# Kernel tuning notes

Hardware: AMD Instinct MI355X
Metric: run time of the kernel (lower is better)

The kernel has to match this reference:

```python
import jax, jax.numpy as jnp
import numpy as np

N, E, G = 50000, 800000, 64
IN, HID, HEADS, OUT = 128, 64, 4, 128
NEG = 0.2  # PyG GATConv default negative_slope


def setup_inputs() -> dict:
    key = jax.random.key(0)
    ks = jax.random.split(key, 12)
    nrm = lambda k, shape, s: (jax.random.normal(k, shape, jnp.float32) * s)
    x = nrm(ks[0], (N, IN), 1.0)
    edge_index = jax.random.randint(ks[1], (2, E), 0, N)
    batch = jnp.sort(jax.random.randint(ks[2], (N,), 0, G))
    W1 = nrm(ks[3], (IN, HEADS * HID), IN ** -0.5)
    a1_src = nrm(ks[4], (HEADS, HID), HID ** -0.5)
    a1_dst = nrm(ks[5], (HEADS, HID), HID ** -0.5)
    b1 = jnp.zeros((HEADS * HID,), jnp.float32)
    W2 = nrm(ks[6], (HEADS * HID, OUT), (HEADS * HID) ** -0.5)
    a2_src = nrm(ks[7], (1, OUT), OUT ** -0.5)
    a2_dst = nrm(ks[8], (1, OUT), OUT ** -0.5)
    b2 = jnp.zeros((OUT,), jnp.float32)
    fc_W = nrm(ks[9], (OUT, OUT), OUT ** -0.5)
    fc_b = jnp.zeros((OUT,), jnp.float32)
    return dict(x=x, edge_index=edge_index, batch=batch, W1=W1, a1_src=a1_src,
                a1_dst=a1_dst, b1=b1, W2=W2, a2_src=a2_src, a2_dst=a2_dst,
                b2=b2, fc_W=fc_W, fc_b=fc_b)


def gat_conv(x, W, a_src, a_dst, b, src, dst, heads):
    n = x.shape[0]
    ch = W.shape[1] // heads
    h = (x @ W).reshape(n, heads, ch)                      # [n, H, C]
    al_s = jnp.einsum('nhc,hc->nh', h, a_src)              # per-node src logits
    al_d = jnp.einsum('nhc,hc->nh', h, a_dst)
    e = al_s[src] + al_d[dst]                              # [E, H]
    e = jnp.where(e > 0, e, NEG * e)                       # LeakyReLU
    # segment softmax over incoming edges of each dst node
    m = jax.lax.stop_gradient(jax.ops.segment_max(e, dst, num_segments=n))
    m = jnp.where(jnp.isfinite(m), m, 0.0)
    ex = jnp.exp(e - m[dst])
    s = jax.ops.segment_sum(ex, dst, num_segments=n)
    alpha = ex / (s[dst] + 1e-16)                          # [E, H]
    out = jax.ops.segment_sum(h[src] * alpha[..., None], dst, num_segments=n)
    return out.reshape(n, heads * ch) + b                  # concat heads + bias


def reference(x, edge_index, batch, W1, a1_src, a1_dst, b1, W2, a2_src, a2_dst, b2, fc_W, fc_b):
    loops = jnp.arange(N, dtype=edge_index.dtype)          # PyG adds self-loops
    src = jnp.concatenate([edge_index[0], loops])
    dst = jnp.concatenate([edge_index[1], loops])
    h = jax.nn.elu(gat_conv(x, W1, a1_src, a1_dst, b1, src, dst, HEADS))
    h = jax.nn.elu(gat_conv(h, W2, a2_src, a2_dst, b2, src, dst, 1))
    sums = jax.ops.segment_sum(h, batch, num_segments=G)
    cnt = jax.ops.segment_sum(jnp.ones((N,), h.dtype), batch, num_segments=G)
    pooled = sums / jnp.maximum(cnt, 1.0)[:, None]         # global mean pool
    return jax.nn.relu(pooled @ fc_W + fc_b)
```

## Files before the change

kernel.cpp:

```cpp
#include <hip/hip_runtime.h>
#include <math.h>

#define N_NODES 50000
#define N_EDGES 800000
#define N_GRAPHS 64
#define NEG 0.2f

typedef unsigned short us;
typedef us us2 __attribute__((ext_vector_type(2)));
typedef us us4 __attribute__((ext_vector_type(4)));
typedef us us8 __attribute__((ext_vector_type(8)));
typedef short bf16x8 __attribute__((ext_vector_type(8)));
typedef float f32x4 __attribute__((ext_vector_type(4)));

__device__ __forceinline__ us bf16rn(float f) {
  unsigned int u = __float_as_uint(f);
  u += 0x7FFFu + ((u >> 16) & 1u);
  return (us)(u >> 16);
}
__device__ __forceinline__ float bf2f(us h) {
  return __uint_as_float(((unsigned int)h) << 16);
}

__global__ __launch_bounds__(256) void convW_kernel(
    const float* __restrict__ W1, const float* __restrict__ W2,
    us* __restrict__ w1h, us* __restrict__ w1l,
    us* __restrict__ w2h, us* __restrict__ w2l) {
  int idx = blockIdx.x * 256 + threadIdx.x;
  const float* W; us *oh, *ol; int K, N, li;
  if (idx < 128 * 256) {
    W = W1; oh = w1h; ol = w1l; K = 128; N = 256; li = idx;
  } else if (idx < 2 * 128 * 256) {
    W = W2; oh = w2h; ol = w2l; K = 256; N = 128; li = idx - 128 * 256;
  } else return;
  int n = li / K, k = li - n * K;
  float f = W[(size_t)k * N + n];
  us h = bf16rn(f);
  oh[li] = h;
  ol[li] = bf16rn(f - bf2f(h));
}

__global__ __launch_bounds__(256, 2) void gemm_bf16x3(
    const float* __restrict__ A, const us* __restrict__ Bth,
    const us* __restrict__ Btl, us* __restrict__ C, int M, int N, int K) {
  __shared__ us Ah[128][40];
  __shared__ us Al[128][40];
  __shared__ us Bh[128][40];
  __shared__ us Bl[128][40];
  int t = threadIdx.x;
  int m0 = blockIdx.x * 128;
  int n0 = blockIdx.y * 128;
  int w = t >> 6, l = t & 63;
  int wr = w >> 1, wc = w & 1;
  int l15 = l & 15, g = l >> 4;

  f32x4 acc[4][4] = {};

  for (int kb = 0; kb < K; kb += 32) {
    #pragma unroll
    for (int i = 0; i < 4; i++) {
      int slot = i * 256 + t;
      int row = slot >> 3, kq = slot & 7;
      float4 v = make_float4(0.f, 0.f, 0.f, 0.f);
      if (m0 + row < M) v = *(const float4*)&A[(size_t)(m0 + row) * K + kb + kq * 4];
      us h0 = bf16rn(v.x), h1 = bf16rn(v.y), h2 = bf16rn(v.z), h3 = bf16rn(v.w);
      us4 hv = {h0, h1, h2, h3};
      us4 lv = {bf16rn(v.x - bf2f(h0)), bf16rn(v.y - bf2f(h1)),
                bf16rn(v.z - bf2f(h2)), bf16rn(v.w - bf2f(h3))};
      *(us4*)&Ah[row][kq * 4] = hv;
      *(us4*)&Al[row][kq * 4] = lv;
    }
    #pragma unroll
    for (int i = 0; i < 2; i++) {
      int slot = i * 256 + t;
      int n = slot >> 2, kq = slot & 3;
      size_t gidx = (size_t)(n0 + n) * K + kb + kq * 8;
      *(us8*)&Bh[n][kq * 8] = *(const us8*)&Bth[gidx];
      *(us8*)&Bl[n][kq * 8] = *(const us8*)&Btl[gidx];
    }
    __syncthreads();

    bf16x8 af[4], al4[4], bf[4], bl4[4];
    #pragma unroll
    for (int i = 0; i < 4; i++) {
      af[i]  = *(const bf16x8*)&Ah[wr * 64 + i * 16 + l15][g * 8];
      al4[i] = *(const bf16x8*)&Al[wr * 64 + i * 16 + l15][g * 8];
      bf[i]  = *(const bf16x8*)&Bh[wc * 64 + i * 16 + l15][g * 8];
      bl4[i] = *(const bf16x8*)&Bl[wc * 64 + i * 16 + l15][g * 8];
    }
    #pragma unroll
    for (int i = 0; i < 4; i++)
      #pragma unroll
      for (int j = 0; j < 4; j++) {
        acc[i][j] = __builtin_amdgcn_mfma_f32_16x16x32_bf16(af[i], bf[j], acc[i][j], 0, 0, 0);
        acc[i][j] = __builtin_amdgcn_mfma_f32_16x16x32_bf16(af[i], bl4[j], acc[i][j], 0, 0, 0);
        acc[i][j] = __builtin_amdgcn_mfma_f32_16x16x32_bf16(al4[i], bf[j], acc[i][j], 0, 0, 0);
      }
    __syncthreads();
  }

  #pragma unroll
  for (int i = 0; i < 4; i++)
    #pragma unroll
    for (int j = 0; j < 4; j++)
      #pragma unroll
      for (int r = 0; r < 4; r++) {
        int row = m0 + wr * 64 + i * 16 + g * 4 + r;
        if (row < M) {
          int col = n0 + wc * 64 + j * 16 + l15;
          C[(size_t)row * N + col] = bf16rn(acc[i][j][r]);
        }
      }
}

__global__ __launch_bounds__(256) void logits1_kernel(
    const us* __restrict__ h1b, const float* __restrict__ a_src,
    const float* __restrict__ a_dst, float* __restrict__ al_s,
    float* __restrict__ al_d) {
  int idx = blockIdx.x * 256 + threadIdx.x;
  if (idx >= N_NODES * 4) return;
  int n = idx >> 2, h = idx & 3;
  const us* hp = &h1b[(size_t)n * 256 + h * 64];
  float ss = 0.f, sd = 0.f;
  #pragma unroll
  for (int i = 0; i < 8; i++) {
    us8 v = *(const us8*)&hp[i * 8];
    #pragma unroll
    for (int j = 0; j < 8; j++) {
      float f = bf2f(v[j]);
      ss += f * a_src[h * 64 + i * 8 + j];
      sd += f * a_dst[h * 64 + i * 8 + j];
    }
  }
  al_s[idx] = ss;
  al_d[idx] = sd;
}

__global__ __launch_bounds__(256) void logits2_kernel(
    const us* __restrict__ h2b, const float* __restrict__ a_src,
    const float* __restrict__ a_dst, float* __restrict__ al_s,
    float* __restrict__ al_d) {
  int n = blockIdx.x * 256 + threadIdx.x;
  if (n >= N_NODES) return;
  const us* hp = &h2b[(size_t)n * 128];
  float ss = 0.f, sd = 0.f;
  #pragma unroll
  for (int i = 0; i < 16; i++) {
    us8 v = *(const us8*)&hp[i * 8];
    #pragma unroll
    for (int j = 0; j < 8; j++) {
      float f = bf2f(v[j]);
      ss += f * a_src[i * 8 + j];
      sd += f * a_dst[i * 8 + j];
    }
  }
  al_s[n] = ss;
  al_d[n] = sd;
}

__global__ __launch_bounds__(256) void count_kernel(const int* __restrict__ dst,
                                                    int* __restrict__ cnt) {
  int e = blockIdx.x * 256 + threadIdx.x;
  if (e < N_EDGES) atomicAdd(&cnt[dst[e]], 1);
}

__global__ __launch_bounds__(256) void scan1_kernel(const int* __restrict__ cnt,
                                                    int* __restrict__ itmp,
                                                    int* __restrict__ bsum) {
  int i = blockIdx.x * 256 + threadIdx.x;
  int v = (i < N_NODES) ? cnt[i] : 0;
  int lane = threadIdx.x & 63, w = threadIdx.x >> 6;
  int s = v;
  #pragma unroll
  for (int off = 1; off < 64; off <<= 1) {
    int tv = __shfl_up(s, off);
    if (lane >= off) s += tv;
  }
  __shared__ int wsum[4];
  if (lane == 63) wsum[w] = s;
  __syncthreads();
  int add = 0;
  for (int p = 0; p < w; p++) add += wsum[p];
  s += add;
  if (i < N_NODES) itmp[i] = s;
  if (threadIdx.x == 255) bsum[blockIdx.x] = s;
}

__global__ __launch_bounds__(256) void scan2_kernel(const int* __restrict__ bsum,
                                                    int* __restrict__ boff,
                                                    int nb) {
  int t = threadIdx.x;
  int v = (t < nb) ? bsum[t] : 0;
  int lane = t & 63, w = t >> 6;
  int s = v;
  #pragma unroll
  for (int off = 1; off < 64; off <<= 1) {
    int tv = __shfl_up(s, off);
    if (lane >= off) s += tv;
  }
  __shared__ int wsum[4];
  if (lane == 63) wsum[w] = s;
  __syncthreads();
  int add = 0;
  for (int p = 0; p < w; p++) add += wsum[p];
  s += add;
  if (t < nb) boff[t] = s - v;
}

__global__ __launch_bounds__(256) void scan3_kernel(const int* __restrict__ cnt,
                                                    const int* __restrict__ itmp,
                                                    const int* __restrict__ boff,
                                                    int* __restrict__ rowst,
                                                    int* __restrict__ cursor) {
  int i = blockIdx.x * 256 + threadIdx.x;
  if (i < N_NODES) {
    int excl = itmp[i] - cnt[i] + boff[i >> 8];
    rowst[i] = excl;
    cursor[i] = excl;
  }
  if (i == 0) rowst[N_NODES] = N_EDGES;
}

__global__ __launch_bounds__(256) void scatter_kernel(
    const int* __restrict__ src, const int* __restrict__ dst,
    int* __restrict__ cursor, int* __restrict__ csr_src) {
  int e = blockIdx.x * 256 + threadIdx.x;
  if (e < N_EDGES) {
    int p = atomicAdd(&cursor[dst[e]], 1);
    csr_src[p] = src[e];
  }
}

__global__ __launch_bounds__(256) void agg1_kernel(
    const us* __restrict__ h1b, const float* __restrict__ al_s,
    const float* __restrict__ al_d, const int* __restrict__ rowst,
    const int* __restrict__ csrc, const float* __restrict__ b1,
    float* __restrict__ out) {
  int d = (blockIdx.x * 256 + threadIdx.x) >> 6;
  int lane = threadIdx.x & 63;
  if (d >= N_NODES) return;
  int head = lane >> 4;
  int c0 = lane * 4;
  int wsel = lane & 48;
  float ald = al_d[d * 4 + head];
  float wsum = 0.f, a0 = 0.f, a1 = 0.f, a2 = 0.f, a3 = 0.f;
  {
    float v = al_s[d * 4 + head] + ald;
    v = v > 0.f ? v : NEG * v;
    float w = __expf(v);
    us4 hv = *(const us4*)&h1b[(size_t)d * 256 + c0];
    wsum += w;
    a0 += w * bf2f(hv[0]); a1 += w * bf2f(hv[1]);
    a2 += w * bf2f(hv[2]); a3 += w * bf2f(hv[3]);
  }
  int beg = rowst[d], end = rowst[d + 1];
  for (int j = beg; j < end; j += 16) {
    int m = end - j;
    m = m < 16 ? m : 16;
    int el = lane & 15;
    int sv = csrc[j + (el < m ? el : 0)];
    float v = al_s[sv * 4 + head] + ald;
    v = v > 0.f ? v : NEG * v;
    float wv = __expf(v);
    #pragma unroll 4
    for (int k = 0; k < m; ++k) {
      int s = __shfl(sv, k);
      float w = __shfl(wv, k + wsel);
      us4 hv = *(const us4*)&h1b[(size_t)s * 256 + c0];
      wsum += w;
      a0 += w * bf2f(hv[0]); a1 += w * bf2f(hv[1]);
      a2 += w * bf2f(hv[2]); a3 += w * bf2f(hv[3]);
    }
  }
  float inv = 1.f / (wsum + 1e-16f);
  float4 bb = *(const float4*)&b1[c0];
  float o0 = a0 * inv + bb.x, o1 = a1 * inv + bb.y;
  float o2 = a2 * inv + bb.z, o3 = a3 * inv + bb.w;
  o0 = o0 > 0.f ? o0 : expm1f(o0);
  o1 = o1 > 0.f ? o1 : expm1f(o1);
  o2 = o2 > 0.f ? o2 : expm1f(o2);
  o3 = o3 > 0.f ? o3 : expm1f(o3);
  *(float4*)&out[(size_t)d * 256 + c0] = make_float4(o0, o1, o2, o3);
}

__global__ __launch_bounds__(256) void agg2_kernel(
    const us* __restrict__ h2b, const float* __restrict__ al_s,
    const float* __restrict__ al_d, const int* __restrict__ rowst,
    const int* __restrict__ csrc, const float* __restrict__ b2,
    float* __restrict__ out) {
  int d = (blockIdx.x * 256 + threadIdx.x) >> 6;
  int lane = threadIdx.x & 63;
  if (d >= N_NODES) return;
  int c0 = lane * 2;
  float ald = al_d[d];
  float wsum = 0.f, a0 = 0.f, a1 = 0.f;
  {
    float v = al_s[d] + ald;
    v = v > 0.f ? v : NEG * v;
    float w = __expf(v);
    us2 hv = *(const us2*)&h2b[(size_t)d * 128 + c0];
    wsum += w;
    a0 += w * bf2f(hv[0]); a1 += w * bf2f(hv[1]);
  }
  int beg = rowst[d], end = rowst[d + 1];
  for (int j = beg; j < end; j += 64) {
    int m = end - j;
    m = m < 64 ? m : 64;
    int sv = csrc[j + (lane < m ? lane : 0)];
    float v = al_s[sv] + ald;
    v = v > 0.f ? v : NEG * v;
    float wv = __expf(v);
    #pragma unroll 4
    for (int k = 0; k < m; ++k) {
      int s = __shfl(sv, k);
      float w = __shfl(wv, k);
      us2 hv = *(const us2*)&h2b[(size_t)s * 128 + c0];
      wsum += w;
      a0 += w * bf2f(hv[0]); a1 += w * bf2f(hv[1]);
    }
  }
  float inv = 1.f / (wsum + 1e-16f);
  float2 bb = *(const float2*)&b2[c0];
  float o0 = a0 * inv + bb.x, o1 = a1 * inv + bb.y;
  o0 = o0 > 0.f ? o0 : expm1f(o0);
  o1 = o1 > 0.f ? o1 : expm1f(o1);
  *(float2*)&out[(size_t)d * 128 + c0] = make_float2(o0, o1);
}

#define PNPB 128
__global__ __launch_bounds__(256) void pool_kernel(const float* __restrict__ y,
                                                   const int* __restrict__ batch,
                                                   float* __restrict__ psum) {
  int t = threadIdx.x;
  int lane32 = t & 31;
  int sub = t >> 5;
  int base = blockIdx.x * PNPB + sub * (PNPB / 8);
  int nend = base + PNPB / 8;
  if (nend > N_NODES) nend = N_NODES;
  float4 acc = make_float4(0.f, 0.f, 0.f, 0.f);
  int curg = -1;
  for (int n = base; n < nend; ++n) {
    int g = batch[n];
    if (g != curg) {
      if (curg >= 0) {
        float* p = &psum[curg * 128 + lane32 * 4];
        atomicAdd(p + 0, acc.x); atomicAdd(p + 1, acc.y);
        atomicAdd(p + 2, acc.z); atomicAdd(p + 3, acc.w);
      }
      acc = make_float4(0.f, 0.f, 0.f, 0.f);
      curg = g;
    }
    float4 v = *(const float4*)&y[(size_t)n * 128 + lane32 * 4];
    acc.x += v.x; acc.y += v.y; acc.z += v.z; acc.w += v.w;
  }
  if (curg >= 0) {
    float* p = &psum[curg * 128 + lane32 * 4];
    atomicAdd(p + 0, acc.x); atomicAdd(p + 1, acc.y);
    atomicAdd(p + 2, acc.z); atomicAdd(p + 3, acc.w);
  }
}

__global__ __launch_bounds__(128) void fc_kernel(
    const float* __restrict__ psum, const int* __restrict__ batch,
    const float* __restrict__ fcW, const float* __restrict__ fcb,
    float* __restrict__ out) {
  __shared__ float pr[128];
  __shared__ int bounds[2];
  int g = blockIdx.x, c = threadIdx.x;
  if (c < 2) {
    int target = g + c;
    int lo = 0, hi = N_NODES;
    while (lo < hi) {
      int mid = (lo + hi) >> 1;
      if (batch[mid] < target) lo = mid + 1; else hi = mid;
    }
    bounds[c] = lo;
  }
  __syncthreads();
  float cnt = (float)(bounds[1] - bounds[0]);
  cnt = cnt > 1.f ? cnt : 1.f;
  pr[c] = psum[g * 128 + c] / cnt;
  __syncthreads();
  float s = fcb[c];
  #pragma unroll 8
  for (int k = 0; k < 128; k++) s += pr[k] * fcW[k * 128 + c];
  out[g * 128 + c] = fmaxf(s, 0.f);
}

extern "C" void kernel_launch(void* const* d_in, const int* in_sizes, int n_in,
                              void* d_out, int out_size, void* d_ws,
                              size_t ws_size, hipStream_t stream) {
  const float* x      = (const float*)d_in[0];
  const int*   ei     = (const int*)d_in[1];
  const int*   batch  = (const int*)d_in[2];
  const float* W1     = (const float*)d_in[3];
  const float* a1_src = (const float*)d_in[4];
  const float* a1_dst = (const float*)d_in[5];
  const float* b1     = (const float*)d_in[6];
  const float* W2     = (const float*)d_in[7];
  const float* a2_src = (const float*)d_in[8];
  const float* a2_dst = (const float*)d_in[9];
  const float* b2     = (const float*)d_in[10];
  const float* fc_W   = (const float*)d_in[11];
  const float* fc_b   = (const float*)d_in[12];
  float* out = (float*)d_out;

  const int* srcp = ei;
  const int* dstp = ei + N_EDGES;
  const int NB = (N_NODES + 255) / 256;

  float* x2   = (float*)d_ws;
  float* y    = x2 + (size_t)N_NODES * 256;
  float* al1s = y + (size_t)N_NODES * 128;
  float* al1d = al1s + N_NODES * 4;
  float* al2s = al1d + N_NODES * 4;
  float* al2d = al2s + N_NODES;
  float* psum = al2d + N_NODES;
  us* h1b  = (us*)(psum + N_GRAPHS * 128);
  us* h2b  = h1b + (size_t)N_NODES * 256;
  us* w1th = h2b + (size_t)N_NODES * 128;
  us* w1tl = w1th + 256 * 128;
  us* w2th = w1tl + 256 * 128;
  us* w2tl = w2th + 128 * 256;
  int* cnt    = (int*)(w2tl + 128 * 256);
  int* bsum   = cnt + N_NODES;
  int* boff   = bsum + 256;
  int* itmp   = boff + 256;
  int* rowst  = itmp + N_NODES;
  int* cursor = rowst + N_NODES + 8;
  int* csrc   = cursor + N_NODES;
  size_t needed = (size_t)((char*)(csrc + N_EDGES) - (char*)d_ws);
  if (ws_size < needed) return;

  hipMemsetAsync(cnt, 0, N_NODES * sizeof(int), stream);
  hipMemsetAsync(psum, 0, N_GRAPHS * 128 * sizeof(float), stream);

  count_kernel<<<(N_EDGES + 255) / 256, 256, 0, stream>>>(dstp, cnt);
  scan1_kernel<<<NB, 256, 0, stream>>>(cnt, itmp, bsum);
  scan2_kernel<<<1, 256, 0, stream>>>(bsum, boff, NB);
  scan3_kernel<<<NB, 256, 0, stream>>>(cnt, itmp, boff, rowst, cursor);
  scatter_kernel<<<(N_EDGES + 255) / 256, 256, 0, stream>>>(srcp, dstp, cursor, csrc);

  convW_kernel<<<(2 * 128 * 256 + 255) / 256, 256, 0, stream>>>(
      W1, W2, w1th, w1tl, w2th, w2tl);

  gemm_bf16x3<<<dim3(391, 2), 256, 0, stream>>>(x, w1th, w1tl, h1b, N_NODES, 256, 128);
  logits1_kernel<<<(N_NODES * 4 + 255) / 256, 256, 0, stream>>>(h1b, a1_src, a1_dst, al1s, al1d);
  agg1_kernel<<<(N_NODES * 64 + 255) / 256, 256, 0, stream>>>(
      h1b, al1s, al1d, rowst, csrc, b1, x2);

  gemm_bf16x3<<<dim3(391, 1), 256, 0, stream>>>(x2, w2th, w2tl, h2b, N_NODES, 128, 256);
  logits2_kernel<<<(N_NODES + 255) / 256, 256, 0, stream>>>(h2b, a2_src, a2_dst, al2s, al2d);
  agg2_kernel<<<(N_NODES * 64 + 255) / 256, 256, 0, stream>>>(
      h2b, al2s, al2d, rowst, csrc, b2, y);

  pool_kernel<<<(N_NODES + PNPB - 1) / PNPB, 256, 0, stream>>>(y, batch, psum);
  fc_kernel<<<N_GRAPHS, 128, 0, stream>>>(psum, batch, fc_W, fc_b, out);
}
```

Baseline: 339.0 us.

## Pre-split GEMM inputs to bf16 hi/lo and batch gather loads in aggregation

The fp32 to bf16 hi/lo split of the GEMM A operand moves out of the GEMM inner loop. For layer 1 a separate xsplit kernel does it, and for layer 2 agg1 now writes bf16 hi/lo directly instead of fp32 x2. The aggregation kernels are restructured to read eight neighbour indices with readlane and issue eight gathers before accumulating, which raises memory-level parallelism. This cuts per-K-block conversion work and the fp32 traffic in the second GEMM, at the cost of an extra pass over x and more registers in the aggregation loops.

Measured after the change: 327.4 us. -3.4%, faster.

```diff
diff --git a/kernel.cpp b/kernel.cpp
--- a/kernel.cpp
+++ b/kernel.cpp
@@ -20,6 +20,24 @@
 }
 __device__ __forceinline__ float bf2f(us h) {
   return __uint_as_float(((unsigned int)h) << 16);
+}
+__device__ __forceinline__ float readlane_f(float v, int l) {
+  return __uint_as_float((unsigned)__builtin_amdgcn_readlane(__float_as_uint(v), l));
+}
+
+__global__ __launch_bounds__(256) void xsplit_kernel(const float* __restrict__ x,
+                                                     us* __restrict__ xh,
+                                                     us* __restrict__ xl,
+                                                     int total4) {
+  int i = blockIdx.x * 256 + threadIdx.x;
+  if (i >= total4) return;
+  float4 v = *(const float4*)&x[(size_t)i * 4];
+  us h0 = bf16rn(v.x), h1 = bf16rn(v.y), h2 = bf16rn(v.z), h3 = bf16rn(v.w);
+  us4 hv = {h0, h1, h2, h3};
+  us4 lv = {bf16rn(v.x - bf2f(h0)), bf16rn(v.y - bf2f(h1)),
+            bf16rn(v.z - bf2f(h2)), bf16rn(v.w - bf2f(h3))};
+  *(us4*)&xh[(size_t)i * 4] = hv;
+  *(us4*)&xl[(size_t)i * 4] = lv;
 }
 
 __global__ __launch_bounds__(256) void convW_kernel(
@@ -41,8 +59,9 @@
 }
 
 __global__ __launch_bounds__(256, 2) void gemm_bf16x3(
-    const float* __restrict__ A, const us* __restrict__ Bth,
-    const us* __restrict__ Btl, us* __restrict__ C, int M, int N, int K) {
+    const us* __restrict__ Agh, const us* __restrict__ Agl,
+    const us* __restrict__ Bth, const us* __restrict__ Btl,
+    us* __restrict__ C, int M, int N, int K) {
   __shared__ us Ah[128][40];
   __shared__ us Al[128][40];
   __shared__ us Bh[128][40];
@@ -57,26 +76,23 @@
   f32x4 acc[4][4] = {};
 
   for (int kb = 0; kb < K; kb += 32) {
-    #pragma unroll
-    for (int i = 0; i < 4; i++) {
+    us8 z = {};
+    #pragma unroll
+    for (int i = 0; i < 2; i++) {
       int slot = i * 256 + t;
-      int row = slot >> 3, kq = slot & 7;
-      float4 v = make_float4(0.f, 0.f, 0.f, 0.f);
-      if (m0 + row < M) v = *(const float4*)&A[(size_t)(m0 + row) * K + kb + kq * 4];
-      us h0 = bf16rn(v.x), h1 = bf16rn(v.y), h2 = bf16rn(v.z), h3 = bf16rn(v.w);
-      us4 hv = {h0, h1, h2, h3};
-      us4 lv = {bf16rn(v.x - bf2f(h0)), bf16rn(v.y - bf2f(h1)),
-                bf16rn(v.z - bf2f(h2)), bf16rn(v.w - bf2f(h3))};
-      *(us4*)&Ah[row][kq * 4] = hv;
-      *(us4*)&Al[row][kq * 4] = lv;
+      int row = slot >> 2, kq = slot & 3;
+      size_t gi = (size_t)(m0 + row) * K + kb + kq * 8;
+      bool ok = (m0 + row) < M;
+      *(us8*)&Ah[row][kq * 8] = ok ? *(const us8*)&Agh[gi] : z;
+      *(us8*)&Al[row][kq * 8] = ok ? *(const us8*)&Agl[gi] : z;
     }
     #pragma unroll
     for (int i = 0; i < 2; i++) {
       int slot = i * 256 + t;
       int n = slot >> 2, kq = slot & 3;
-      size_t gidx = (size_t)(n0 + n) * K + kb + kq * 8;
-      *(us8*)&Bh[n][kq * 8] = *(const us8*)&Bth[gidx];
-      *(us8*)&Bl[n][kq * 8] = *(const us8*)&Btl[gidx];
+      size_t gi = (size_t)(n0 + n) * K + kb + kq * 8;
+      *(us8*)&Bh[n][kq * 8] = *(const us8*)&Bth[gi];
+      *(us8*)&Bl[n][kq * 8] = *(const us8*)&Btl[gi];
     }
     __syncthreads();
 
@@ -235,7 +251,7 @@
     const us* __restrict__ h1b, const float* __restrict__ al_s,
     const float* __restrict__ al_d, const int* __restrict__ rowst,
     const int* __restrict__ csrc, const float* __restrict__ b1,
-    float* __restrict__ out) {
+    us* __restrict__ outh, us* __restrict__ outl) {
   int d = (blockIdx.x * 256 + threadIdx.x) >> 6;
   int lane = threadIdx.x & 63;
   if (d >= N_NODES) return;
@@ -254,33 +270,72 @@
     a2 += w * bf2f(hv[2]); a3 += w * bf2f(hv[3]);
   }
   int beg = rowst[d], end = rowst[d + 1];
-  for (int j = beg; j < end; j += 16) {
-    int m = end - j;
-    m = m < 16 ? m : 16;
+  int j = beg;
+  for (; j + 16 <= end; j += 16) {
+    int el = lane & 15;
+    int sv = csrc[j + el];
+    float v = al_s[sv * 4 + head] + ald;
+    v = v > 0.f ? v : NEG * v;
+    float wv = __expf(v);
+    #pragma unroll
+    for (int half = 0; half < 2; ++half) {
+      int ss[8]; us4 hv[8];
+      #pragma unroll
+      for (int k = 0; k < 8; ++k)
+        ss[k] = __builtin_amdgcn_readlane(sv, half * 8 + k);
+      #pragma unroll
+      for (int k = 0; k < 8; ++k)
+        hv[k] = *(const us4*)&h1b[(size_t)(unsigned)ss[k] * 256 + c0];
+      #pragma unroll
+      for (int k = 0; k < 8; ++k) {
+        float w = __shfl(wv, half * 8 + k + wsel);
+        wsum += w;
+        a0 += w * bf2f(hv[k][0]); a1 += w * bf2f(hv[k][1]);
+        a2 += w * bf2f(hv[k][2]); a3 += w * bf2f(hv[k][3]);
+      }
+    }
+  }
+  int m = end - j;
+  if (m > 0) {
     int el = lane & 15;
     int sv = csrc[j + (el < m ? el : 0)];
     float v = al_s[sv * 4 + head] + ald;
     v = v > 0.f ? v : NEG * v;
     float wv = __expf(v);
-    #pragma unroll 4
-    for (int k = 0; k < m; ++k) {
-      int s = __shfl(sv, k);
-      float w = __shfl(wv, k + wsel);
-      us4 hv = *(const us4*)&h1b[(size_t)s * 256 + c0];
-      wsum += w;
-      a0 += w * bf2f(hv[0]); a1 += w * bf2f(hv[1]);
-      a2 += w * bf2f(hv[2]); a3 += w * bf2f(hv[3]);
+    for (int b = 0; b < m; b += 8) {
+      int ss[8]; us4 hv[8];
+      #pragma unroll
+      for (int k = 0; k < 8; ++k) {
+        int kk = b + k;
+        ss[k] = __builtin_amdgcn_readlane(sv, kk < m ? kk : 0);
+      }
+      #pragma unroll
+      for (int k = 0; k < 8; ++k)
+        hv[k] = *(const us4*)&h1b[(size_t)(unsigned)ss[k] * 256 + c0];
+      #pragma unroll
+      for (int k = 0; k < 8; ++k) {
+        int kk = b + k;
+        float w = __shfl(wv, (kk < m ? kk : 0) + wsel);
+        if (kk >= m) w = 0.f;
+        wsum += w;
+        a0 += w * bf2f(hv[k][0]); a1 += w * bf2f(hv[k][1]);
+        a2 += w * bf2f(hv[k][2]); a3 += w * bf2f(hv[k][3]);
+      }
     }
   }
   float inv = 1.f / (wsum + 1e-16f);
   float4 bb = *(const float4*)&b1[c0];
-  float o0 = a0 * inv + bb.x, o1 = a1 * inv + bb.y;
-  float o2 = a2 * inv + bb.z, o3 = a3 * inv + bb.w;
-  o0 = o0 > 0.f ? o0 : expm1f(o0);
-  o1 = o1 > 0.f ? o1 : expm1f(o1);
-  o2 = o2 > 0.f ? o2 : expm1f(o2);
-  o3 = o3 > 0.f ? o3 : expm1f(o3);
-  *(float4*)&out[(size_t)d * 256 + c0] = make_float4(o0, o1, o2, o3);
+  float o[4] = {a0 * inv + bb.x, a1 * inv + bb.y, a2 * inv + bb.z, a3 * inv + bb.w};
+  us4 oh, ol;
+  #pragma unroll
+  for (int i = 0; i < 4; i++) {
+    float e = o[i] > 0.f ? o[i] : expm1f(o[i]);
+    us h = bf16rn(e);
+    oh[i] = h;
+    ol[i] = bf16rn(e - bf2f(h));
+  }
+  *(us4*)&outh[(size_t)d * 256 + c0] = oh;
+  *(us4*)&outl[(size_t)d * 256 + c0] = ol;
 }
 
 __global__ __launch_bounds__(256) void agg2_kernel(
@@ -310,13 +365,24 @@
     float v = al_s[sv] + ald;
     v = v > 0.f ? v : NEG * v;
     float wv = __expf(v);
-    #pragma unroll 4
-    for (int k = 0; k < m; ++k) {
-      int s = __shfl(sv, k);
-      float w = __shfl(wv, k);
-      us2 hv = *(const us2*)&h2b[(size_t)s * 128 + c0];
-      wsum += w;
-      a0 += w * bf2f(hv[0]); a1 += w * bf2f(hv[1]);
+    for (int b = 0; b < m; b += 8) {
+      int ss[8]; us2 hv[8];
+      #pragma unroll
+      for (int k = 0; k < 8; ++k) {
+        int kk = b + k;
+        ss[k] = __builtin_amdgcn_readlane(sv, kk < m ? kk : 0);
+      }
+      #pragma unroll
+      for (int k = 0; k < 8; ++k)
+        hv[k] = *(const us2*)&h2b[(size_t)(unsigned)ss[k] * 128 + c0];
+      #pragma unroll
+      for (int k = 0; k < 8; ++k) {
+        int kk = b + k;
+        float w = readlane_f(wv, kk < m ? kk : 0);
+        if (kk >= m) w = 0.f;
+        wsum += w;
+        a0 += w * bf2f(hv[k][0]); a1 += w * bf2f(hv[k][1]);
+      }
     }
   }
   float inv = 1.f / (wsum + 1e-16f);
@@ -409,14 +475,17 @@
   const int* dstp = ei + N_EDGES;
   const int NB = (N_NODES + 255) / 256;
 
-  float* x2   = (float*)d_ws;
-  float* y    = x2 + (size_t)N_NODES * 256;
+  float* y    = (float*)d_ws;
   float* al1s = y + (size_t)N_NODES * 128;
   float* al1d = al1s + N_NODES * 4;
   float* al2s = al1d + N_NODES * 4;
   float* al2d = al2s + N_NODES;
   float* psum = al2d + N_NODES;
-  us* h1b  = (us*)(psum + N_GRAPHS * 128);
+  us* xh   = (us*)(psum + N_GRAPHS * 128);
+  us* xl   = xh + (size_t)N_NODES * 128;
+  us* x2h  = xl + (size_t)N_NODES * 128;
+  us* x2l  = x2h + (size_t)N_NODES * 256;
+  us* h1b  = x2l + (size_t)N_NODES * 256;
   us* h2b  = h1b + (size_t)N_NODES * 256;
   us* w1th = h2b + (size_t)N_NODES * 128;
   us* w1tl = w1th + 256 * 128;
@@ -441,15 +510,17 @@
   scan3_kernel<<<NB, 256, 0, stream>>>(cnt, itmp, boff, rowst, cursor);
   scatter_kernel<<<(N_EDGES + 255) / 256, 256, 0, stream>>>(srcp, dstp, cursor, csrc);
 
+  xsplit_kernel<<<(N_NODES * 128 / 4 + 255) / 256, 256, 0, stream>>>(
+      x, xh, xl, N_NODES * 128 / 4);
   convW_kernel<<<(2 * 128 * 256 + 255) / 256, 256, 0, stream>>>(
       W1, W2, w1th, w1tl, w2th, w2tl);
 
-  gemm_bf16x3<<<dim3(391, 2), 256, 0, stream>>>(x, w1th, w1tl, h1b, N_NODES, 256, 128);
+  gemm_bf16x3<<<dim3(391, 2), 256, 0, stream>>>(xh, xl, w1th, w1tl, h1b, N_NODES, 256, 128);
   logits1_kernel<<<(N_NODES * 4 + 255) / 256, 256, 0, stream>>>(h1b, a1_src, a1_dst, al1s, al1d);
   agg1_kernel<<<(N_NODES * 64 + 255) / 256, 256, 0, stream>>>(
-      h1b, al1s, al1d, rowst, csrc, b1, x2);
-
-  gemm_bf16x3<<<dim3(391, 1), 256, 0, stream>>>(x2, w2th, w2tl, h2b, N_NODES, 128, 256);
+      h1b, al1s, al1d, rowst, csrc, b1, x2h, x2l);
+
+  gemm_bf16x3<<<dim3(391, 1), 256, 0, stream>>>(x2h, x2l, w2th, w2tl, h2b, N_NODES, 128, 256);
   logits2_kernel<<<(N_NODES + 255) / 256, 256, 0, stream>>>(h2b, a2_src, a2_dst, al2s, al2d);
   agg2_kernel<<<(N_NODES * 64 + 255) / 256, 256, 0, stream>>>(
       h2b, al2s, al2d, rowst, csrc, b2, y);
```
